# Kernel tuning notes

Hardware: AMD Instinct MI355X
Metric: run time of the kernel (lower is better)

The kernel has to match this reference:

```python
import jax, jax.numpy as jnp
import numpy as np

N_STATIONS = 100000
N_TIME = 365
N_NEIGHBORS = 5
SMOOTHING = 0.1


def setup_inputs() -> dict:
    key = jax.random.key(0)
    k = jax.random.split(key, 6)
    N, T, K = N_STATIONS, N_TIME, N_NEIGHBORS
    time_vector = jnp.arange(T, dtype=jnp.float32) / 365.25  # years
    constant_offset = jax.random.normal(k[0], (N,), jnp.float32) * 10.0
    linear_trend = jax.random.normal(k[1], (N,), jnp.float32) * 5.0  # mm/yr (ps00_rates buffer)
    seasonal_amplitudes = jax.random.uniform(k[2], (N, 4), jnp.float32) * 6.0
    seasonal_phases = jax.random.uniform(k[3], (N, 4), jnp.float32) * (2.0 * np.pi)
    neighbor_indices = jax.random.randint(k[4], (N, K), 0, N)
    w = jax.random.uniform(k[5], (N, K), jnp.float32) + 1e-3
    neighbor_weights = w / jnp.sum(w, axis=1, keepdims=True)  # row-normalized, like exp-dist weights
    periods = jnp.array([0.25, 0.5, 1.0, 2.0], dtype=jnp.float32)
    return {
        'time_vector': time_vector,
        'constant_offset': constant_offset,
        'linear_trend': linear_trend,
        'seasonal_amplitudes': seasonal_amplitudes,
        'seasonal_phases': seasonal_phases,
        'neighbor_weights': neighbor_weights,
        'periods': periods,
        'neighbor_indices': neighbor_indices,
    }


def _smooth(p, neighbor_indices, neighbor_weights):
    # p: [N, 4]; vectorized version of per-station loop: gather + weighted mean
    nb = p[neighbor_indices]                                   # [N, K, 4]
    avg = jnp.einsum('nkf,nk->nf', nb, neighbor_weights)       # [N, 4]
    return (1.0 - SMOOTHING) * p + SMOOTHING * avg


def reference(time_vector, constant_offset, linear_trend, seasonal_amplitudes,
              seasonal_phases, neighbor_weights, periods, neighbor_indices):
    amps = _smooth(seasonal_amplitudes, neighbor_indices, neighbor_weights)   # [N, 4]
    phs = _smooth(seasonal_phases, neighbor_indices, neighbor_weights)        # [N, 4]
    t = time_vector[None, :]                                                  # [1, T]
    signals = constant_offset[:, None] + linear_trend[:, None] * t           # [N, T]
    two_pi = jnp.float32(2.0 * np.pi)
    for f in range(4):  # fixed small set of seasonal periods
        freq = 1.0 / periods[f]
        signals = signals + amps[:, f:f + 1] * jnp.sin(two_pi * freq * t + phs[:, f:f + 1])
    return signals
```

## Files before the change

kernel.cpp:

```cpp
#include <hip/hip_runtime.h>
#include <math.h>

typedef float f32x2 __attribute__((ext_vector_type(2)));

#define TWO_PI 6.283185307179586f
#define SMOOTH 0.1f
#define SPW 16
#define WAVES 4
#define BLOCK 256
#define SPB (SPW * WAVES)
#define NPAIR 3

__device__ __forceinline__ f32x2 sp2(float x) { f32x2 r; r.x = x; r.y = x; return r; }
__device__ __forceinline__ void store8(float* p, f32x2 v) { __builtin_memcpy(p, &v, 8); }

__global__ __launch_bounds__(BLOCK) void fused_v4(
    const float* __restrict__ time_vector,
    const float* __restrict__ constant_offset,
    const float* __restrict__ linear_trend,
    const float* __restrict__ amps,
    const float* __restrict__ phs,
    const float* __restrict__ wgt,
    const float* __restrict__ periods,
    const int*   __restrict__ nbidx,
    float* __restrict__ out,
    int N, int T, int K)
{
    __shared__ float lc[SPB][12];

    const int tid   = threadIdx.x;
    const int wave  = tid >> 6;
    const int lane  = tid & 63;
    const int wbase = blockIdx.x * SPB + wave * SPW;

    int send = N - wbase; if (send > SPW) send = SPW;
    if (send <= 0) return;

    const bool p1 = (lane < SPW) && (wbase + lane) < N;
    if (p1) {
        const int i = wbase + lane;
        float4 a = reinterpret_cast<const float4*>(amps)[i];
        float4 p = reinterpret_cast<const float4*>(phs)[i];

        int   nb[5]; float w[5];
        __builtin_memcpy(nb, nbidx + (size_t)i * K, 5 * sizeof(int));
        __builtin_memcpy(w,  wgt   + (size_t)i * K, 5 * sizeof(float));

        float av0 = 0.f, av1 = 0.f, av2 = 0.f, av3 = 0.f;
        float pv0 = 0.f, pv1 = 0.f, pv2 = 0.f, pv3 = 0.f;
        #pragma unroll
        for (int k = 0; k < 5; ++k) {
            float4 na = reinterpret_cast<const float4*>(amps)[nb[k]];
            float4 np = reinterpret_cast<const float4*>(phs)[nb[k]];
            av0 += w[k] * na.x; av1 += w[k] * na.y; av2 += w[k] * na.z; av3 += w[k] * na.w;
            pv0 += w[k] * np.x; pv1 += w[k] * np.y; pv2 += w[k] * np.z; pv3 += w[k] * np.w;
        }
        float sa0 = (1.0f - SMOOTH) * a.x + SMOOTH * av0;
        float sa1 = (1.0f - SMOOTH) * a.y + SMOOTH * av1;
        float sa2 = (1.0f - SMOOTH) * a.z + SMOOTH * av2;
        float sa3 = (1.0f - SMOOTH) * a.w + SMOOTH * av3;
        float sp0 = (1.0f - SMOOTH) * p.x + SMOOTH * pv0;
        float sp1 = (1.0f - SMOOTH) * p.y + SMOOTH * pv1;
        float sp2 = (1.0f - SMOOTH) * p.z + SMOOTH * pv2;
        float sp3 = (1.0f - SMOOTH) * p.w + SMOOTH * pv3;

        float s0f = __sinf(sp0), c0f = __cosf(sp0);
        float s1f = __sinf(sp1), c1f = __cosf(sp1);
        float s2f = __sinf(sp2), c2f = __cosf(sp2);
        float s3f = __sinf(sp3), c3f = __cosf(sp3);

        const int row = wave * SPW + lane;
        float4 vA, vB; float2 vC;
        vA.x = constant_offset[i]; vA.y = linear_trend[i];
        vA.z = sa0 * c0f;  vA.w = sa0 * s0f;
        vB.x = sa1 * c1f;  vB.y = sa1 * s1f;
        vB.z = sa2 * c2f;  vB.w = sa2 * s2f;
        vC.x = sa3 * c3f;  vC.y = sa3 * s3f;
        *reinterpret_cast<float4*>(&lc[row][0]) = vA;
        *reinterpret_cast<float4*>(&lc[row][4]) = vB;
        *reinterpret_cast<float2*>(&lc[row][8]) = vC;
    }

    const float w0 = TWO_PI / periods[0];
    const float w1 = TWO_PI / periods[1];
    const float w2 = TWO_PI / periods[2];
    const float w3 = TWO_PI / periods[3];

    f32x2 tv[NPAIR];
    f32x2 bs[NPAIR][4], bc[NPAIR][4];
    bool full[NPAIR], any[NPAIR];
    const int t0 = 2 * lane;

    #pragma unroll
    for (int p = 0; p < NPAIR; ++p) {
        const int t = t0 + 128 * p;
        const bool v0 = (t < T), v1 = (t + 1 < T);
        any[p] = v0; full[p] = v1;
        float ta = v0 ? time_vector[t]     : 0.f;
        float tb = v1 ? time_vector[t + 1] : 0.f;
        f32x2 tvp; tvp.x = ta; tvp.y = tb;
        tv[p] = tvp;
        #pragma unroll
        for (int f = 0; f < 4; ++f) {
            const float wf = (f == 0) ? w0 : (f == 1) ? w1 : (f == 2) ? w2 : w3;
            f32x2 s, c;
            s.x = __sinf(wf * ta); s.y = __sinf(wf * tb);
            c.x = __cosf(wf * ta); c.y = __cosf(wf * tb);
            bs[p][f] = s; bc[p][f] = c;
        }
    }

    asm volatile("s_waitcnt lgkmcnt(0)" ::: "memory");
    __builtin_amdgcn_sched_barrier(0);
    __builtin_amdgcn_wave_barrier();

    const float* lcw   = &lc[wave * SPW][0];
    float*       obase = out + (size_t)wbase * T;

    #pragma unroll 4
    for (int j = 0; j < send; ++j) {
        const float* cf = lcw + j * 12;
        float4 cA = *reinterpret_cast<const float4*>(cf);
        float4 cB = *reinterpret_cast<const float4*>(cf + 4);
        float2 cC = *reinterpret_cast<const float2*>(cf + 8);
        float* orow = obase + (size_t)j * T;

        #pragma unroll
        for (int p = 0; p < NPAIR; ++p) {
            f32x2 sig = sp2(cA.x) + sp2(cA.y) * tv[p];
            sig += sp2(cA.z) * bs[p][0] + sp2(cA.w) * bc[p][0];
            sig += sp2(cB.x) * bs[p][1] + sp2(cB.y) * bc[p][1];
            sig += sp2(cB.z) * bs[p][2] + sp2(cB.w) * bc[p][2];
            sig += sp2(cC.x) * bs[p][3] + sp2(cC.y) * bc[p][3];
            const int t = t0 + 128 * p;
            if (full[p])      store8(orow + t, sig);
            else if (any[p])  orow[t] = sig.x;
        }
    }
}

extern "C" void kernel_launch(void* const* d_in, const int* in_sizes, int n_in,
                              void* d_out, int out_size, void* d_ws, size_t ws_size,
                              hipStream_t stream)
{
    const float* time_vector     = (const float*)d_in[0];
    const float* constant_offset = (const float*)d_in[1];
    const float* linear_trend    = (const float*)d_in[2];
    const float* amps            = (const float*)d_in[3];
    const float* phs             = (const float*)d_in[4];
    const float* wgt             = (const float*)d_in[5];
    const float* periods         = (const float*)d_in[6];
    const int*   nbidx           = (const int*)d_in[7];

    int T = in_sizes[0];
    int N = in_sizes[1];
    int K = in_sizes[5] / N;
    float* out = (float*)d_out;

    int grid = (N + SPB - 1) / SPB;
    fused_v4<<<grid, BLOCK, 0, stream>>>(
        time_vector, constant_offset, linear_trend, amps, phs, wgt,
        periods, nbidx, out, N, T, K);
}
```

Before: 39.34 us.

## Broadcast per-station coefficients via readlane instead of LDS, halve stations per wave

Each station's smoothed coefficients stay in registers and are broadcast to the whole wave with v_readlane/SGPR reads, which replaces the LDS staging, waitcnt and wave barrier. Stations per wave drop from 16 to 8, so the grid doubles and the per-wave loop can be fully unrolled with compile-time lane indices. In exchange, every wave recomputes the time-basis sin/cos table for only 8 output rows, so that fixed cost is spread over half as many rows, and the redundant lanes clamp to valid station IDs and repeat the gather work.

Result: slower. 40.29 us (+2.4%).

```diff
diff --git a/kernel.cpp b/kernel.cpp
--- a/kernel.cpp
+++ b/kernel.cpp
@@ -5,7 +5,7 @@
 
 #define TWO_PI 6.283185307179586f
 #define SMOOTH 0.1f
-#define SPW 16
+#define SPW 8
 #define WAVES 4
 #define BLOCK 256
 #define SPB (SPW * WAVES)
@@ -13,8 +13,11 @@
 
 __device__ __forceinline__ f32x2 sp2(float x) { f32x2 r; r.x = x; r.y = x; return r; }
 __device__ __forceinline__ void store8(float* p, f32x2 v) { __builtin_memcpy(p, &v, 8); }
+__device__ __forceinline__ float rlane(float v, int l) {
+    return __uint_as_float((unsigned)__builtin_amdgcn_readlane((int)__float_as_uint(v), l));
+}
 
-__global__ __launch_bounds__(BLOCK) void fused_v4(
+__global__ __launch_bounds__(BLOCK) void fused_v5(
     const float* __restrict__ time_vector,
     const float* __restrict__ constant_offset,
     const float* __restrict__ linear_trend,
@@ -26,60 +29,48 @@
     float* __restrict__ out,
     int N, int T, int K)
 {
-    __shared__ float lc[SPB][12];
-
     const int tid   = threadIdx.x;
     const int wave  = tid >> 6;
     const int lane  = tid & 63;
     const int wbase = blockIdx.x * SPB + wave * SPW;
 
+    if (wbase >= N) return;
     int send = N - wbase; if (send > SPW) send = SPW;
-    if (send <= 0) return;
 
-    const bool p1 = (lane < SPW) && (wbase + lane) < N;
-    if (p1) {
-        const int i = wbase + lane;
-        float4 a = reinterpret_cast<const float4*>(amps)[i];
-        float4 p = reinterpret_cast<const float4*>(phs)[i];
+    int sid = wbase + (lane & (SPW - 1));
+    if (sid >= N) sid = N - 1;
 
-        int   nb[5]; float w[5];
-        __builtin_memcpy(nb, nbidx + (size_t)i * K, 5 * sizeof(int));
-        __builtin_memcpy(w,  wgt   + (size_t)i * K, 5 * sizeof(float));
+    float4 a = reinterpret_cast<const float4*>(amps)[sid];
+    float4 p = reinterpret_cast<const float4*>(phs)[sid];
 
-        float av0 = 0.f, av1 = 0.f, av2 = 0.f, av3 = 0.f;
-        float pv0 = 0.f, pv1 = 0.f, pv2 = 0.f, pv3 = 0.f;
-        #pragma unroll
-        for (int k = 0; k < 5; ++k) {
-            float4 na = reinterpret_cast<const float4*>(amps)[nb[k]];
-            float4 np = reinterpret_cast<const float4*>(phs)[nb[k]];
-            av0 += w[k] * na.x; av1 += w[k] * na.y; av2 += w[k] * na.z; av3 += w[k] * na.w;
-            pv0 += w[k] * np.x; pv1 += w[k] * np.y; pv2 += w[k] * np.z; pv3 += w[k] * np.w;
-        }
-        float sa0 = (1.0f - SMOOTH) * a.x + SMOOTH * av0;
-        float sa1 = (1.0f - SMOOTH) * a.y + SMOOTH * av1;
-        float sa2 = (1.0f - SMOOTH) * a.z + SMOOTH * av2;
-        float sa3 = (1.0f - SMOOTH) * a.w + SMOOTH * av3;
-        float sp0 = (1.0f - SMOOTH) * p.x + SMOOTH * pv0;
-        float sp1 = (1.0f - SMOOTH) * p.y + SMOOTH * pv1;
-        float sp2 = (1.0f - SMOOTH) * p.z + SMOOTH * pv2;
-        float sp3 = (1.0f - SMOOTH) * p.w + SMOOTH * pv3;
+    int   nb[5]; float w[5];
+    __builtin_memcpy(nb, nbidx + (size_t)sid * K, 5 * sizeof(int));
+    __builtin_memcpy(w,  wgt   + (size_t)sid * K, 5 * sizeof(float));
 
-        float s0f = __sinf(sp0), c0f = __cosf(sp0);
-        float s1f = __sinf(sp1), c1f = __cosf(sp1);
-        float s2f = __sinf(sp2), c2f = __cosf(sp2);
-        float s3f = __sinf(sp3), c3f = __cosf(sp3);
+    float av0 = 0.f, av1 = 0.f, av2 = 0.f, av3 = 0.f;
+    float pv0 = 0.f, pv1 = 0.f, pv2 = 0.f, pv3 = 0.f;
+    #pragma unroll
+    for (int k = 0; k < 5; ++k) {
+        float4 na = reinterpret_cast<const float4*>(amps)[nb[k]];
+        float4 np = reinterpret_cast<const float4*>(phs)[nb[k]];
+        av0 += w[k] * na.x; av1 += w[k] * na.y; av2 += w[k] * na.z; av3 += w[k] * na.w;
+        pv0 += w[k] * np.x; pv1 += w[k] * np.y; pv2 += w[k] * np.z; pv3 += w[k] * np.w;
+    }
+    float sa0 = (1.0f - SMOOTH) * a.x + SMOOTH * av0;
+    float sa1 = (1.0f - SMOOTH) * a.y + SMOOTH * av1;
+    float sa2 = (1.0f - SMOOTH) * a.z + SMOOTH * av2;
+    float sa3 = (1.0f - SMOOTH) * a.w + SMOOTH * av3;
+    float sp0 = (1.0f - SMOOTH) * p.x + SMOOTH * pv0;
+    float sp1 = (1.0f - SMOOTH) * p.y + SMOOTH * pv1;
+    float sp2v = (1.0f - SMOOTH) * p.z + SMOOTH * pv2;
+    float sp3 = (1.0f - SMOOTH) * p.w + SMOOTH * pv3;
 
-        const int row = wave * SPW + lane;
-        float4 vA, vB; float2 vC;
-        vA.x = constant_offset[i]; vA.y = linear_trend[i];
-        vA.z = sa0 * c0f;  vA.w = sa0 * s0f;
-        vB.x = sa1 * c1f;  vB.y = sa1 * s1f;
-        vB.z = sa2 * c2f;  vB.w = sa2 * s2f;
-        vC.x = sa3 * c3f;  vC.y = sa3 * s3f;
-        *reinterpret_cast<float4*>(&lc[row][0]) = vA;
-        *reinterpret_cast<float4*>(&lc[row][4]) = vB;
-        *reinterpret_cast<float2*>(&lc[row][8]) = vC;
-    }
+    float cc = constant_offset[sid];
+    float cm = linear_trend[sid];
+    float cA0 = sa0 * __cosf(sp0),  cB0 = sa0 * __sinf(sp0);
+    float cA1 = sa1 * __cosf(sp1),  cB1 = sa1 * __sinf(sp1);
+    float cA2 = sa2 * __cosf(sp2v), cB2 = sa2 * __sinf(sp2v);
+    float cA3 = sa3 * __cosf(sp3),  cB3 = sa3 * __sinf(sp3);
 
     const float w0 = TWO_PI / periods[0];
     const float w1 = TWO_PI / periods[1];
@@ -92,49 +83,46 @@
     const int t0 = 2 * lane;
 
     #pragma unroll
-    for (int p = 0; p < NPAIR; ++p) {
-        const int t = t0 + 128 * p;
+    for (int q = 0; q < NPAIR; ++q) {
+        const int t = t0 + 128 * q;
         const bool v0 = (t < T), v1 = (t + 1 < T);
-        any[p] = v0; full[p] = v1;
+        any[q] = v0; full[q] = v1;
         float ta = v0 ? time_vector[t]     : 0.f;
         float tb = v1 ? time_vector[t + 1] : 0.f;
         f32x2 tvp; tvp.x = ta; tvp.y = tb;
-        tv[p] = tvp;
+        tv[q] = tvp;
         #pragma unroll
         for (int f = 0; f < 4; ++f) {
             const float wf = (f == 0) ? w0 : (f == 1) ? w1 : (f == 2) ? w2 : w3;
             f32x2 s, c;
             s.x = __sinf(wf * ta); s.y = __sinf(wf * tb);
             c.x = __cosf(wf * ta); c.y = __cosf(wf * tb);
-            bs[p][f] = s; bc[p][f] = c;
+            bs[q][f] = s; bc[q][f] = c;
         }
     }
 
-    asm volatile("s_waitcnt lgkmcnt(0)" ::: "memory");
-    __builtin_amdgcn_sched_barrier(0);
-    __builtin_amdgcn_wave_barrier();
+    float* obase = out + (size_t)wbase * T;
 
-    const float* lcw   = &lc[wave * SPW][0];
-    float*       obase = out + (size_t)wbase * T;
-
-    #pragma unroll 4
-    for (int j = 0; j < send; ++j) {
-        const float* cf = lcw + j * 12;
-        float4 cA = *reinterpret_cast<const float4*>(cf);
-        float4 cB = *reinterpret_cast<const float4*>(cf + 4);
-        float2 cC = *reinterpret_cast<const float2*>(cf + 8);
+    #pragma unroll
+    for (int j = 0; j < SPW; ++j) {
+        if (j >= send) break;
+        float sc  = rlane(cc,  j), sm  = rlane(cm,  j);
+        float sA0 = rlane(cA0, j), sB0 = rlane(cB0, j);
+        float sA1 = rlane(cA1, j), sB1 = rlane(cB1, j);
+        float sA2 = rlane(cA2, j), sB2 = rlane(cB2, j);
+        float sA3 = rlane(cA3, j), sB3 = rlane(cB3, j);
         float* orow = obase + (size_t)j * T;
 
         #pragma unroll
-        for (int p = 0; p < NPAIR; ++p) {
-            f32x2 sig = sp2(cA.x) + sp2(cA.y) * tv[p];
-            sig += sp2(cA.z) * bs[p][0] + sp2(cA.w) * bc[p][0];
-            sig += sp2(cB.x) * bs[p][1] + sp2(cB.y) * bc[p][1];
-            sig += sp2(cB.z) * bs[p][2] + sp2(cB.w) * bc[p][2];
-            sig += sp2(cC.x) * bs[p][3] + sp2(cC.y) * bc[p][3];
-            const int t = t0 + 128 * p;
-            if (full[p])      store8(orow + t, sig);
-            else if (any[p])  orow[t] = sig.x;
+        for (int q = 0; q < NPAIR; ++q) {
+            f32x2 sig = sp2(sc) + sp2(sm) * tv[q];
+            sig += sp2(sA0) * bs[q][0] + sp2(sB0) * bc[q][0];
+            sig += sp2(sA1) * bs[q][1] + sp2(sB1) * bc[q][1];
+            sig += sp2(sA2) * bs[q][2] + sp2(sB2) * bc[q][2];
+            sig += sp2(sA3) * bs[q][3] + sp2(sB3) * bc[q][3];
+            const int t = t0 + 128 * q;
+            if (full[q])      store8(orow + t, sig);
+            else if (any[q])  orow[t] = sig.x;
         }
     }
 }
@@ -158,7 +146,7 @@
     float* out = (float*)d_out;
 
     int grid = (N + SPB - 1) / SPB;
-    fused_v4<<<grid, BLOCK, 0, stream>>>(
+    fused_v5<<<grid, BLOCK, 0, stream>>>(
         time_vector, constant_offset, linear_trend, amps, phs, wgt,
         periods, nbidx, out, N, T, K);
 }
```
